# Optimization experiments

Hardware: AMD Instinct MI355X
Metric: run time of the kernel (lower is better)

## Reference

```python
import jax, jax.numpy as jnp
import numpy as np

N = 8192      # total nodes (32 graphs x 256 nodes)
B = 32        # graphs in batch
E = 65536     # edges per graph (avg degree 16)
DK = 512      # d_k = d_v
H = 32        # mlp / conv channel width
VB = 2048     # body visual dim
VF = 512      # face visual dim
EPS = 1e-5


def setup_inputs() -> dict:
    key = jax.random.key(0)
    ks = jax.random.split(key, 26)
    def n(k, sh, s=1.0):
        return jax.random.normal(k, sh, dtype=jnp.float32) * s
    s2, s512, s32 = 1.0 / np.sqrt(2.0), 1.0 / np.sqrt(512.0), 1.0 / np.sqrt(32.0)
    inp = {}
    inp["x"] = n(ks[0], (N, 2))
    inp["visual_body"] = n(ks[1], (N, VB))
    inp["visual_face"] = n(ks[2], (N, VF))
    # attention projections (no bias)
    inp["Wq"] = n(ks[3], (2, DK), s2)
    inp["Wk"] = n(ks[4], (2, DK), s2)
    inp["Wv"] = n(ks[5], (2, DK), s2)
    # input_mlp: LayerNorm(512) -> PReLU -> Linear(512,32)
    inp["ln_g"] = jnp.ones((DK,), jnp.float32)
    inp["ln_b"] = jnp.zeros((DK,), jnp.float32)
    inp["prelu_a"] = jnp.float32(0.25)
    inp["mlp_W"] = n(ks[6], (DK, H), s512)
    inp["mlp_b"] = jnp.zeros((H,), jnp.float32)
    # node projection Linear(32,1)
    inp["np_W"] = n(ks[7], (H, 1), s32)
    inp["np_b"] = jnp.zeros((1,), jnp.float32)
    # CMCosConv linear weights (32->32) for body / face
    inp["body_W"] = n(ks[8], (H, H), s32)
    inp["body_b"] = jnp.zeros((H,), jnp.float32)
    inp["face_W"] = n(ks[9], (H, H), s32)
    inp["face_b"] = jnp.zeros((H,), jnp.float32)
    # gcn projections Linear(32,1)
    inp["pb_W"] = n(ks[10], (H, 1), s32)
    inp["pb_b"] = jnp.zeros((1,), jnp.float32)
    inp["pf_W"] = n(ks[11], (H, 1), s32)
    inp["pf_b"] = jnp.zeros((1,), jnp.float32)
    # int-valued graph structure
    inp["edge_index_body"] = jax.random.randint(ks[12], (2, E), 0, N)
    inp["edge_index_face"] = jax.random.randint(ks[13], (2, E), 0, N)
    inp["batch_vec"] = jnp.arange(N, dtype=jnp.int64) // (N // B)  # 32 graphs, 256 nodes each
    return inp


def cmcos_conv(x, edge_index, visual, W, b):
    # per-edge cosine(visual_src, visual_dst) * Linear(x_src), scatter-sum to dst
    src, dst = edge_index[0], edge_index[1]
    h = x @ W + b                                          # [N, H]
    vn = visual * jax.lax.rsqrt(jnp.sum(visual * visual, -1, keepdims=True) + 1e-8)
    w = jnp.sum(vn[src] * vn[dst], axis=-1)                # [E] cosine edge weights
    msg = w[:, None] * h[src]                              # [E, H]
    return jax.ops.segment_sum(msg, dst, num_segments=x.shape[0])


def reference(x, visual_body, visual_face, Wq, Wk, Wv, ln_g, ln_b, prelu_a,
              mlp_W, mlp_b, np_W, np_b, body_W, body_b, face_W, face_b,
              pb_W, pb_b, pf_W, pf_b, edge_index_body, edge_index_face, batch_vec):
    sz_b = int(batch_vec[-1]) + 1
    q = (x @ Wq).reshape(sz_b, -1, DK)
    k = (x @ Wk).reshape(sz_b, -1, DK)
    v = (x @ Wv).reshape(sz_b, -1, DK)
    attn = jax.nn.softmax(jnp.einsum('bqd,bkd->bqk', q, k) / np.sqrt(DK), axis=-1)
    out = jnp.einsum('bqk,bkd->bqd', attn, v).reshape(-1, DK)   # [N, 512]
    # input_mlp: LayerNorm -> PReLU -> Linear (dropout is identity in eval)
    mu = jnp.mean(out, -1, keepdims=True)
    var = jnp.mean((out - mu) ** 2, -1, keepdims=True)
    h = (out - mu) * jax.lax.rsqrt(var + EPS) * ln_g + ln_b
    h = jnp.where(h >= 0, h, prelu_a * h)
    h = h @ mlp_W + mlp_b                                       # [N, 32]
    nodes_scores = (h @ np_W + np_b)[:, 0]
    hb = cmcos_conv(h, edge_index_body, visual_body, body_W, body_b)
    hf = cmcos_conv(h, edge_index_face, visual_face, face_W, face_b)
    gcn_scores_body = (hb @ pb_W + pb_b)[:, 0]
    gcn_scores_face = (hf @ pf_W + pf_b)[:, 0]
    return nodes_scores + gcn_scores_body + gcn_scores_face
```

## Files before the change

kernel.cpp:

```cpp
#include <hip/hip_runtime.h>

#define NN 8192
#define NB 32
#define NG 256
#define NE 65536
#define DK 512
#define HC 32
#define DB 2048
#define DF 512

#define BODY_DW (NN*DB/4)
#define FACE_DW (NN*DF/4)
#define B_BODY (BODY_DW/2048)
#define B_FACE (FACE_DW/2048)
#define B_FILL 512
#define SLOTS  40
#define QSCALE 16.0f

typedef float v4f __attribute__((ext_vector_type(4)));

#if __has_builtin(__builtin_amdgcn_sdot4)
#define HW_SDOT 1
#else
#define HW_SDOT 0
#endif

__device__ __forceinline__ unsigned pack4_i8(float4 v) {
    const float M = 12582912.0f;
    unsigned b0 = __float_as_uint(fmaf(v.x, QSCALE, M));
    unsigned b1 = __float_as_uint(fmaf(v.y, QSCALE, M));
    unsigned b2 = __float_as_uint(fmaf(v.z, QSCALE, M));
    unsigned b3 = __float_as_uint(fmaf(v.w, QSCALE, M));
    return (b0 & 255u) | ((b1 & 255u) << 8) | ((b2 & 255u) << 16) | ((b3 & 255u) << 24);
}
__device__ __forceinline__ int sdot4(int a, int b, int c) {
#if HW_SDOT
    return __builtin_amdgcn_sdot4(a, b, c, false);
#else
    c += (int)(signed char)(a)       * (int)(signed char)(b);
    c += (int)(signed char)(a >> 8)  * (int)(signed char)(b >> 8);
    c += (int)(signed char)(a >> 16) * (int)(signed char)(b >> 16);
    c += (int)(signed char)(a >> 24) * (int)(signed char)(b >> 24);
    return c;
#endif
}
__device__ __forceinline__ int dot16(int4 a, int4 b, int c) {
    c = sdot4(a.x, b.x, c);
    c = sdot4(a.y, b.y, c);
    c = sdot4(a.z, b.z, c);
    c = sdot4(a.w, b.w, c);
    return c;
}
__device__ __forceinline__ float d4(float4 v) {
    return v.x*v.x + v.y*v.y + v.z*v.z + v.w*v.w;
}
__device__ __forceinline__ v4f prelu4(v4f nd, float alpha) {
    v4f r;
    r.x = (nd.x >= 0.f) ? nd.x : alpha*nd.x;
    r.y = (nd.y >= 0.f) ? nd.y : alpha*nd.y;
    r.z = (nd.z >= 0.f) ? nd.z : alpha*nd.z;
    r.w = (nd.w >= 0.f) ? nd.w : alpha*nd.w;
    return r;
}

struct Params {
    const float *vb, *vf, *x, *Wq, *Wk, *Wv, *ln_g, *ln_b, *prelu_a;
    const float *mlp_W, *mlp_b, *np_W, *np_b, *body_W, *body_b, *face_W, *face_b;
    const float *pb_W, *pb_b, *pf_W, *pf_b;
    const int *eib, *eif;
    unsigned *vnb, *vnf;
    float *invb, *invf;
    float *a_ws, *cb, *cf, *fused;
    float *mvec;
    int *counts, *bkt;
    float *out;
};

__global__ __launch_bounds__(256) void k1_kernel(Params p) {
    __shared__ float2 xs[NG];
    __shared__ float pm[4][4];
    __shared__ float sm4[4];
    __shared__ float rss[16];
    __shared__ float wred[4][8];
    __shared__ float fs_np[HC], fs_fb[HC], fs_ff[HC];
    const int bid = blockIdx.x, tid = threadIdx.x;
    const int lane = tid & 63, wave = tid >> 6;

    if (bid < NB) {
        const int gg = bid;
        xs[tid] = ((const float2*)p.x)[gg*NG + tid];
        const int d = tid * 2;
        float q0a = p.Wq[d],    q0b = p.Wq[d+1];
        float q1a = p.Wq[DK+d], q1b = p.Wq[DK+d+1];
        float k0a = p.Wk[d],    k0b = p.Wk[d+1];
        float k1a = p.Wk[DK+d], k1b = p.Wk[DK+d+1];
        float m00 = q0a*k0a + q0b*k0b;
        float m01 = q0a*k1a + q0b*k1b;
        float m10 = q1a*k0a + q1b*k0b;
        float m11 = q1a*k1a + q1b*k1b;
        #pragma unroll
        for (int off = 32; off > 0; off >>= 1) {
            m00 += __shfl_down(m00,off); m01 += __shfl_down(m01,off);
            m10 += __shfl_down(m10,off); m11 += __shfl_down(m11,off);
        }
        if (lane == 0) { pm[wave][0]=m00; pm[wave][1]=m01; pm[wave][2]=m10; pm[wave][3]=m11; }
        __syncthreads();
        if (tid < 4) sm4[tid] = pm[0][tid] + pm[1][tid] + pm[2][tid] + pm[3][tid];
        __syncthreads();
        const float scale = 0.04419417382415922f;
        const float2 xi = xs[tid];
        const float u0 = (xi.x*sm4[0] + xi.y*sm4[2]) * scale;
        const float u1 = (xi.x*sm4[1] + xi.y*sm4[3]) * scale;
        float m = -1e30f;
        for (int j = 0; j < NG; j++) m = fmaxf(m, u0*xs[j].x + u1*xs[j].y);
        float S = 0.f, a0 = 0.f, a1 = 0.f;
        for (int j = 0; j < NG; j++) {
            float2 xj = xs[j];
            float pr = __expf(u0*xj.x + u1*xj.y - m);
            S += pr; a0 += pr*xj.x; a1 += pr*xj.y;
        }
        const float invS = 1.f / S;
        ((float2*)p.a_ws)[gg*NG + tid] = make_float2(a0*invS, a1*invS);
        return;
    }
    if (bid == NB) {
        {
            const int d = tid * 2;
            float u0 = p.Wv[d], u1 = p.Wv[d+1];
            float w0 = p.Wv[DK+d], w1 = p.Wv[DK+d+1];
            float s0 = u0 + u1, s1 = w0 + w1;
            float q00 = u0*u0 + u1*u1, q01 = u0*w0 + u1*w1, q11 = w0*w0 + w1*w1;
            #pragma unroll
            for (int off = 1; off < 64; off <<= 1) {
                s0 += __shfl_xor(s0,off); s1 += __shfl_xor(s1,off);
                q00 += __shfl_xor(q00,off); q01 += __shfl_xor(q01,off); q11 += __shfl_xor(q11,off);
            }
            if (lane == 0) {
                wred[wave][0]=s0; wred[wave][1]=s1; wred[wave][2]=q00; wred[wave][3]=q01; wred[wave][4]=q11;
            }
        }
        if (tid < HC) {
            float sB = 0.f, sF = 0.f;
            #pragma unroll 8
            for (int c = 0; c < HC; c++) {
                sB += p.body_W[tid*HC + c] * p.pb_W[c];
                sF += p.face_W[tid*HC + c] * p.pf_W[c];
            }
            fs_fb[tid] = sB; fs_ff[tid] = sF;
            fs_np[tid] = p.np_W[tid];
        } else if (tid == HC) {
            float s = 0.f;
            for (int c = 0; c < HC; c++) s += p.body_b[c] * p.pb_W[c];
            p.fused[64] = s;
        } else if (tid == HC + 1) {
            float s = 0.f;
            for (int c = 0; c < HC; c++) s += p.face_b[c] * p.pf_W[c];
            p.fused[65] = s;
        }
        __syncthreads();
        if (tid < 5) p.fused[66+tid] = wred[0][tid]+wred[1][tid]+wred[2][tid]+wred[3][tid];
        #pragma unroll
        for (int rr = tid; rr < DK; rr += 256) {
            const float* row = p.mlp_W + rr*HC;
            float dnp = 0.f, db = 0.f, df = 0.f;
            #pragma unroll 8
            for (int c = 0; c < HC; c++) {
                float w = row[c];
                dnp += w * fs_np[c]; db += w * fs_fb[c]; df += w * fs_ff[c];
            }
            p.mvec[rr] = dnp; p.mvec[DK + rr] = db; p.mvec[2*DK + rr] = df;
        }
        if (tid < 3) {
            const float* fv = (tid == 0) ? fs_np : (tid == 1) ? fs_fb : fs_ff;
            float s = 0.f;
            for (int c = 0; c < HC; c++) s += p.mlp_b[c] * fv[c];
            p.mvec[3*DK + tid] = s;
        }
        return;
    }
    if (bid == NB + 1) {
        int4 z = {0, 0, 0, 0};
        int4* c4 = (int4*)p.counts;
        #pragma unroll
        for (int i = 0; i < (2*NN/4)/256; i++) c4[i*256 + tid] = z;
        return;
    }
    {
        const int pb = bid - (NB + 2);
        const bool body = pb < B_BODY;
        const float4* __restrict__ src = body ? (const float4*)p.vb : (const float4*)p.vf;
        unsigned* __restrict__ dst = body ? p.vnb : p.vnf;
        const int base = (body ? pb : pb - B_BODY) * 2048 + tid;
        if (tid < 16) rss[tid] = 0.f;
        __syncthreads();
        float4 v0 = src[base];
        float4 v1 = src[base + 256];
        float4 v2 = src[base + 512];
        float4 v3 = src[base + 768];
        float4 v4 = src[base + 1024];
        float4 v5 = src[base + 1280];
        float4 v6 = src[base + 1536];
        float4 v7 = src[base + 1792];
        __builtin_amdgcn_sched_barrier(0);
        dst[base]        = pack4_i8(v0);
        dst[base + 256]  = pack4_i8(v1);
        dst[base + 512]  = pack4_i8(v2);
        dst[base + 768]  = pack4_i8(v3);
        dst[base + 1024] = pack4_i8(v4);
        dst[base + 1280] = pack4_i8(v5);
        dst[base + 1536] = pack4_i8(v6);
        dst[base + 1792] = pack4_i8(v7);
        if (body) {
            float sq[4];
            sq[0] = d4(v0) + d4(v1);
            sq[1] = d4(v2) + d4(v3);
            sq[2] = d4(v4) + d4(v5);
            sq[3] = d4(v6) + d4(v7);
            #pragma unroll
            for (int r = 0; r < 4; r++) {
                float ss = sq[r];
                #pragma unroll
                for (int off = 32; off > 0; off >>= 1) ss += __shfl_xor(ss, off);
                if (lane == 0) atomicAdd(&rss[r], ss);
            }
            __syncthreads();
            if (tid < 4) p.invb[pb*4 + tid] = rsqrtf(rss[tid] + 1e-8f);
        } else {
            float sq[8] = {d4(v0), d4(v1), d4(v2), d4(v3), d4(v4), d4(v5), d4(v6), d4(v7)};
            #pragma unroll
            for (int j = 0; j < 8; j++) {
                float ss = sq[j];
                #pragma unroll
                for (int off = 32; off > 0; off >>= 1) ss += __shfl_xor(ss, off);
                if (lane == 0) atomicAdd(&rss[(wave >> 1) + 2*j], ss);
            }
            __syncthreads();
            if (tid < 16) p.invf[(pb - B_BODY)*16 + tid] = rsqrtf(rss[tid] + 1e-8f);
        }
    }
}

__global__ __launch_bounds__(256) void k2_kernel(Params p) {
    const int bid = blockIdx.x, tid = threadIdx.x;
    const int wave = tid >> 6, lane = tid & 63;

    if (bid < B_FILL) {
        const int e = bid * 256 + tid;
        if (e < NE) {
            int s = p.eib[e], d = p.eib[NE + e];
            int slot = atomicAdd(&p.counts[d], 1);
            if (slot < SLOTS) p.bkt[d*SLOTS + slot] = s;
        } else {
            int e2 = e - NE;
            int s = p.eif[e2], d = p.eif[NE + e2];
            int slot = atomicAdd(&p.counts[NN + d], 1);
            if (slot < SLOTS) p.bkt[(NN + d)*SLOTS + slot] = s;
        }
        return;
    }
    const int node = (bid - B_FILL) * 4 + wave;
    const float a0 = p.a_ws[node*2], a1 = p.a_ws[node*2+1];
    const float s0 = p.fused[66], s1 = p.fused[67];
    const float q00 = p.fused[68], q01 = p.fused[69], q11 = p.fused[70];
    const float mean = (a0*s0 + a1*s1) * (1.f/DK);
    const float msq  = (a0*a0*q00 + 2.f*a0*a1*q01 + a1*a1*q11) * (1.f/DK);
    const float inv  = rsqrtf(msq - mean*mean + 1e-5f);
    const float alpha = p.prelu_a[0];

    const v4f* wv0 = (const v4f*)p.Wv;
    const v4f* wv1 = (const v4f*)(p.Wv + DK);
    const v4f* g4 = (const v4f*)p.ln_g;
    const v4f* b4 = (const v4f*)p.ln_b;
    const v4f* mnp = (const v4f*)p.mvec;
    const v4f* mb  = (const v4f*)(p.mvec + DK);
    const v4f* mf  = (const v4f*)(p.mvec + 2*DK);

    const int c4 = lane * 2;
    v4f t0 = prelu4((a0*wv0[c4]   + a1*wv1[c4]   - mean) * inv * g4[c4]   + b4[c4],   alpha);
    v4f t1 = prelu4((a0*wv0[c4+1] + a1*wv1[c4+1] - mean) * inv * g4[c4+1] + b4[c4+1], alpha);

    v4f q0 = t0*mnp[c4] + t1*mnp[c4+1];
    v4f q1 = t0*mb[c4]  + t1*mb[c4+1];
    v4f q2 = t0*mf[c4]  + t1*mf[c4+1];
    float d0 = (q0.x+q0.y) + (q0.z+q0.w);
    float d1 = (q1.x+q1.y) + (q1.z+q1.w);
    float d2 = (q2.x+q2.y) + (q2.z+q2.w);
    #pragma unroll
    for (int off = 1; off < 64; off <<= 1) {
        d0 += __shfl_xor(d0, off);
        d1 += __shfl_xor(d1, off);
        d2 += __shfl_xor(d2, off);
    }
    if (lane == 0) {
        const float qinv2 = 1.0f / (QSCALE * QSCALE);
        p.out[node] = d0 + p.mvec[3*DK] + p.np_b[0] + p.pb_b[0] + p.pf_b[0];
        p.cb[node] = (d1 + p.mvec[3*DK+1] + p.fused[64]) * qinv2 * p.invb[node];
        p.cf[node] = (d2 + p.mvec[3*DK+2] + p.fused[65]) * qinv2 * p.invf[node];
    }
}

__global__ __launch_bounds__(256) void scat_kernel(Params p) {
    const int wave = threadIdx.x >> 6, lane = threadIdx.x & 63;
    const bool body = blockIdx.x < NN/4;
    const int node = (body ? blockIdx.x : blockIdx.x - NN/4) * 4 + wave;
    float acc = 0.f;
    if (body) {
        const int cnt = min(p.counts[node], SLOTS);
        const int* bkt = p.bkt + node*SLOTS;
        const int4* D = (const int4*)(p.vnb + (size_t)node * (DB/4));
        int4 d0 = D[lane], d1 = D[lane + 64];
        for (int i = 0; i < cnt; i += 4) {
            const int4 bi = *(const int4*)(bkt + i);
            const int sA = bi.x;
            const int sB = (i+1 < cnt) ? bi.y : node;
            const int sC = (i+2 < cnt) ? bi.z : node;
            const int sD = (i+3 < cnt) ? bi.w : node;
            const float cA = p.cb[sA];
            const float cB = (i+1 < cnt) ? p.cb[sB] : 0.f;
            const float cC = (i+2 < cnt) ? p.cb[sC] : 0.f;
            const float cD = (i+3 < cnt) ? p.cb[sD] : 0.f;
            const int4* A0 = (const int4*)(p.vnb + (size_t)sA * (DB/4));
            const int4* A1 = (const int4*)(p.vnb + (size_t)sB * (DB/4));
            const int4* A2 = (const int4*)(p.vnb + (size_t)sC * (DB/4));
            const int4* A3 = (const int4*)(p.vnb + (size_t)sD * (DB/4));
            int4 a00 = A0[lane], a01 = A0[lane + 64];
            int4 a10 = A1[lane], a11 = A1[lane + 64];
            int4 a20 = A2[lane], a21 = A2[lane + 64];
            int4 a30 = A3[lane], a31 = A3[lane + 64];
            __builtin_amdgcn_sched_barrier(0);
            int x0 = dot16(a01, d1, dot16(a00, d0, 0));
            int x1 = dot16(a11, d1, dot16(a10, d0, 0));
            int x2 = dot16(a21, d1, dot16(a20, d0, 0));
            int x3 = dot16(a31, d1, dot16(a30, d0, 0));
            acc += (float)x0*cA + (float)x1*cB + (float)x2*cC + (float)x3*cD;
        }
        #pragma unroll
        for (int off = 1; off < 64; off <<= 1) acc += __shfl_xor(acc, off);
        if (lane == 0) atomicAdd(&p.out[node], acc * p.invb[node]);
    } else {
        const int cnt = min(p.counts[NN + node], SLOTS);
        const int* bkt = p.bkt + (size_t)(NN + node)*SLOTS;
        const int2* D = (const int2*)(p.vnf + (size_t)node * (DF/4));
        int2 dd = D[lane];
        for (int i = 0; i < cnt; i += 4) {
            const int4 bi = *(const int4*)(bkt + i);
            const int sA = bi.x;
            const int sB = (i+1 < cnt) ? bi.y : node;
            const int sC = (i+2 < cnt) ? bi.z : node;
            const int sD = (i+3 < cnt) ? bi.w : node;
            const float cA = p.cf[sA];
            const float cB = (i+1 < cnt) ? p.cf[sB] : 0.f;
            const float cC = (i+2 < cnt) ? p.cf[sC] : 0.f;
            const float cD = (i+3 < cnt) ? p.cf[sD] : 0.f;
            const int2* A0 = (const int2*)(p.vnf + (size_t)sA * (DF/4));
            const int2* A1 = (const int2*)(p.vnf + (size_t)sB * (DF/4));
            const int2* A2 = (const int2*)(p.vnf + (size_t)sC * (DF/4));
            const int2* A3 = (const int2*)(p.vnf + (size_t)sD * (DF/4));
            int2 a0 = A0[lane];
            int2 a1 = A1[lane];
            int2 a2 = A2[lane];
            int2 a3 = A3[lane];
            __builtin_amdgcn_sched_barrier(0);
            int x0 = sdot4(a0.y, dd.y, sdot4(a0.x, dd.x, 0));
            int x1 = sdot4(a1.y, dd.y, sdot4(a1.x, dd.x, 0));
            int x2 = sdot4(a2.y, dd.y, sdot4(a2.x, dd.x, 0));
            int x3 = sdot4(a3.y, dd.y, sdot4(a3.x, dd.x, 0));
            acc += (float)x0*cA + (float)x1*cB + (float)x2*cC + (float)x3*cD;
        }
        #pragma unroll
        for (int off = 1; off < 64; off <<= 1) acc += __shfl_xor(acc, off);
        if (lane == 0) atomicAdd(&p.out[node], acc * p.invf[node]);
    }
}

extern "C" void kernel_launch(void* const* d_in, const int* in_sizes, int n_in,
                              void* d_out, int out_size, void* d_ws, size_t ws_size,
                              hipStream_t stream) {
    char* ws = (char*)d_ws;
    size_t off = 0;
    auto alloc = [&](size_t bytes) { void* pp = ws + off; off += (bytes + 15) & ~size_t(15); return pp; };

    Params p;
    p.vb      = (const float*)d_in[1];
    p.vf      = (const float*)d_in[2];
    p.x       = (const float*)d_in[0];
    p.Wq      = (const float*)d_in[3];
    p.Wk      = (const float*)d_in[4];
    p.Wv      = (const float*)d_in[5];
    p.ln_g    = (const float*)d_in[6];
    p.ln_b    = (const float*)d_in[7];
    p.prelu_a = (const float*)d_in[8];
    p.mlp_W   = (const float*)d_in[9];
    p.mlp_b   = (const float*)d_in[10];
    p.np_W    = (const float*)d_in[11];
    p.np_b    = (const float*)d_in[12];
    p.body_W  = (const float*)d_in[13];
    p.body_b  = (const float*)d_in[14];
    p.face_W  = (const float*)d_in[15];
    p.face_b  = (const float*)d_in[16];
    p.pb_W    = (const float*)d_in[17];
    p.pb_b    = (const float*)d_in[18];
    p.pf_W    = (const float*)d_in[19];
    p.pf_b    = (const float*)d_in[20];
    p.eib     = (const int*)d_in[21];
    p.eif     = (const int*)d_in[22];
    p.vnb     = (unsigned*)alloc((size_t)BODY_DW*4);
    p.vnf     = (unsigned*)alloc((size_t)FACE_DW*4);
    p.invb    = (float*)alloc((size_t)NN*4);
    p.invf    = (float*)alloc((size_t)NN*4);
    p.a_ws    = (float*)alloc((size_t)NN*2*4);
    p.cb      = (float*)alloc((size_t)NN*4);
    p.cf      = (float*)alloc((size_t)NN*4);
    p.fused   = (float*)alloc((size_t)72*4);
    p.mvec    = (float*)alloc((size_t)1544*4);
    p.counts  = (int*)alloc((size_t)2*NN*4);
    p.bkt     = (int*)alloc((size_t)2*NN*SLOTS*4);
    p.out     = (float*)d_out;

    k1_kernel<<<NB + 2 + B_BODY + B_FACE, 256, 0, stream>>>(p);
    k2_kernel<<<B_FILL + NN/4, 256, 0, stream>>>(p);
    scat_kernel<<<NN/2, 256, 0, stream>>>(p);
}
```

Baseline: 191.6 us.

## Move edge bucketing into k1 and compute row norms from quantized int8 values

```diff
diff --git a/kernel.cpp b/kernel.cpp
--- a/kernel.cpp
+++ b/kernel.cpp
@@ -50,9 +50,6 @@
     c = sdot4(a.z, b.z, c);
     c = sdot4(a.w, b.w, c);
     return c;
-}
-__device__ __forceinline__ float d4(float4 v) {
-    return v.x*v.x + v.y*v.y + v.z*v.z + v.w*v.w;
 }
 __device__ __forceinline__ v4f prelu4(v4f nd, float alpha) {
     v4f r;
@@ -80,7 +77,7 @@
     __shared__ float2 xs[NG];
     __shared__ float pm[4][4];
     __shared__ float sm4[4];
-    __shared__ float rss[16];
+    __shared__ int rss[16];
     __shared__ float wred[4][8];
     __shared__ float fs_np[HC], fs_fb[HC], fs_ff[HC];
     const int bid = blockIdx.x, tid = threadIdx.x;
@@ -178,20 +175,27 @@
         }
         return;
     }
-    if (bid == NB + 1) {
-        int4 z = {0, 0, 0, 0};
-        int4* c4 = (int4*)p.counts;
-        #pragma unroll
-        for (int i = 0; i < (2*NN/4)/256; i++) c4[i*256 + tid] = z;
+    if (bid < NB + 1 + B_FILL) {
+        const int e = (bid - (NB + 1)) * 256 + tid;
+        if (e < NE) {
+            int s = p.eib[e], d = p.eib[NE + e];
+            int slot = atomicAdd(&p.counts[d], 1);
+            if (slot < SLOTS) p.bkt[d*SLOTS + slot] = s;
+        } else {
+            int e2 = e - NE;
+            int s = p.eif[e2], d = p.eif[NE + e2];
+            int slot = atomicAdd(&p.counts[NN + d], 1);
+            if (slot < SLOTS) p.bkt[(NN + d)*SLOTS + slot] = s;
+        }
         return;
     }
     {
-        const int pb = bid - (NB + 2);
+        const int pb = bid - (NB + 1 + B_FILL);
         const bool body = pb < B_BODY;
         const float4* __restrict__ src = body ? (const float4*)p.vb : (const float4*)p.vf;
         unsigned* __restrict__ dst = body ? p.vnb : p.vnf;
         const int base = (body ? pb : pb - B_BODY) * 2048 + tid;
-        if (tid < 16) rss[tid] = 0.f;
+        if (tid < 16) rss[tid] = 0;
         __syncthreads();
         float4 v0 = src[base];
         float4 v1 = src[base + 256];
@@ -202,63 +206,60 @@
         float4 v6 = src[base + 1536];
         float4 v7 = src[base + 1792];
         __builtin_amdgcn_sched_barrier(0);
-        dst[base]        = pack4_i8(v0);
-        dst[base + 256]  = pack4_i8(v1);
-        dst[base + 512]  = pack4_i8(v2);
-        dst[base + 768]  = pack4_i8(v3);
-        dst[base + 1024] = pack4_i8(v4);
-        dst[base + 1280] = pack4_i8(v5);
-        dst[base + 1536] = pack4_i8(v6);
-        dst[base + 1792] = pack4_i8(v7);
+        unsigned q0 = pack4_i8(v0);
+        unsigned q1 = pack4_i8(v1);
+        unsigned q2 = pack4_i8(v2);
+        unsigned q3 = pack4_i8(v3);
+        unsigned q4 = pack4_i8(v4);
+        unsigned q5 = pack4_i8(v5);
+        unsigned q6 = pack4_i8(v6);
+        unsigned q7 = pack4_i8(v7);
+        dst[base]        = q0;
+        dst[base + 256]  = q1;
+        dst[base + 512]  = q2;
+        dst[base + 768]  = q3;
+        dst[base + 1024] = q4;
+        dst[base + 1280] = q5;
+        dst[base + 1536] = q6;
+        dst[base + 1792] = q7;
         if (body) {
-            float sq[4];
-            sq[0] = d4(v0) + d4(v1);
-            sq[1] = d4(v2) + d4(v3);
-            sq[2] = d4(v4) + d4(v5);
-            sq[3] = d4(v6) + d4(v7);
+            int sq[4];
+            sq[0] = sdot4((int)q1, (int)q1, sdot4((int)q0, (int)q0, 0));
+            sq[1] = sdot4((int)q3, (int)q3, sdot4((int)q2, (int)q2, 0));
+            sq[2] = sdot4((int)q5, (int)q5, sdot4((int)q4, (int)q4, 0));
+            sq[3] = sdot4((int)q7, (int)q7, sdot4((int)q6, (int)q6, 0));
             #pragma unroll
             for (int r = 0; r < 4; r++) {
-                float ss = sq[r];
+                int ss = sq[r];
                 #pragma unroll
                 for (int off = 32; off > 0; off >>= 1) ss += __shfl_xor(ss, off);
                 if (lane == 0) atomicAdd(&rss[r], ss);
             }
             __syncthreads();
-            if (tid < 4) p.invb[pb*4 + tid] = rsqrtf(rss[tid] + 1e-8f);
+            if (tid < 4) p.invb[pb*4 + tid] = rsqrtf((float)rss[tid] + 1.0f);
         } else {
-            float sq[8] = {d4(v0), d4(v1), d4(v2), d4(v3), d4(v4), d4(v5), d4(v6), d4(v7)};
+            int sq[8] = {sdot4((int)q0,(int)q0,0), sdot4((int)q1,(int)q1,0),
+                         sdot4((int)q2,(int)q2,0), sdot4((int)q3,(int)q3,0),
+                         sdot4((int)q4,(int)q4,0), sdot4((int)q5,(int)q5,0),
+                         sdot4((int)q6,(int)q6,0), sdot4((int)q7,(int)q7,0)};
             #pragma unroll
             for (int j = 0; j < 8; j++) {
-                float ss = sq[j];
+                int ss = sq[j];
                 #pragma unroll
                 for (int off = 32; off > 0; off >>= 1) ss += __shfl_xor(ss, off);
                 if (lane == 0) atomicAdd(&rss[(wave >> 1) + 2*j], ss);
             }
             __syncthreads();
-            if (tid < 16) p.invf[(pb - B_BODY)*16 + tid] = rsqrtf(rss[tid] + 1e-8f);
+            if (tid < 16) p.invf[(pb - B_BODY)*16 + tid] = rsqrtf((float)rss[tid] + 1.0f);
         }
     }
 }
 
 __global__ __launch_bounds__(256) void k2_kernel(Params p) {
-    const int bid = blockIdx.x, tid = threadIdx.x;
+    const int tid = threadIdx.x;
     const int wave = tid >> 6, lane = tid & 63;
-
-    if (bid < B_FILL) {
-        const int e = bid * 256 + tid;
-        if (e < NE) {
-            int s = p.eib[e], d = p.eib[NE + e];
-            int slot = atomicAdd(&p.counts[d], 1);
-            if (slot < SLOTS) p.bkt[d*SLOTS + slot] = s;
-        } else {
-            int e2 = e - NE;
-            int s = p.eif[e2], d = p.eif[NE + e2];
-            int slot = atomicAdd(&p.counts[NN + d], 1);
-            if (slot < SLOTS) p.bkt[(NN + d)*SLOTS + slot] = s;
-        }
-        return;
-    }
-    const int node = (bid - B_FILL) * 4 + wave;
+    const int node = blockIdx.x * 4 + wave;
+
     const float a0 = p.a_ws[node*2], a1 = p.a_ws[node*2+1];
     const float s0 = p.fused[66], s1 = p.fused[67];
     const float q00 = p.fused[68], q01 = p.fused[69], q11 = p.fused[70];
@@ -279,12 +280,12 @@
     v4f t0 = prelu4((a0*wv0[c4]   + a1*wv1[c4]   - mean) * inv * g4[c4]   + b4[c4],   alpha);
     v4f t1 = prelu4((a0*wv0[c4+1] + a1*wv1[c4+1] - mean) * inv * g4[c4+1] + b4[c4+1], alpha);
 
-    v4f q0 = t0*mnp[c4] + t1*mnp[c4+1];
-    v4f q1 = t0*mb[c4]  + t1*mb[c4+1];
-    v4f q2 = t0*mf[c4]  + t1*mf[c4+1];
-    float d0 = (q0.x+q0.y) + (q0.z+q0.w);
-    float d1 = (q1.x+q1.y) + (q1.z+q1.w);
-    float d2 = (q2.x+q2.y) + (q2.z+q2.w);
+    v4f w0 = t0*mnp[c4] + t1*mnp[c4+1];
+    v4f w1 = t0*mb[c4]  + t1*mb[c4+1];
+    v4f w2 = t0*mf[c4]  + t1*mf[c4+1];
+    float d0 = (w0.x+w0.y) + (w0.z+w0.w);
+    float d1 = (w1.x+w1.y) + (w1.z+w1.w);
+    float d2 = (w2.x+w2.y) + (w2.z+w2.w);
     #pragma unroll
     for (int off = 1; off < 64; off <<= 1) {
         d0 += __shfl_xor(d0, off);
@@ -292,10 +293,9 @@
         d2 += __shfl_xor(d2, off);
     }
     if (lane == 0) {
-        const float qinv2 = 1.0f / (QSCALE * QSCALE);
         p.out[node] = d0 + p.mvec[3*DK] + p.np_b[0] + p.pb_b[0] + p.pf_b[0];
-        p.cb[node] = (d1 + p.mvec[3*DK+1] + p.fused[64]) * qinv2 * p.invb[node];
-        p.cf[node] = (d2 + p.mvec[3*DK+2] + p.fused[65]) * qinv2 * p.invf[node];
+        p.cb[node] = (d1 + p.mvec[3*DK+1] + p.fused[64]) * p.invb[node];
+        p.cf[node] = (d2 + p.mvec[3*DK+2] + p.fused[65]) * p.invf[node];
     }
 }
 
@@ -417,7 +417,8 @@
     p.bkt     = (int*)alloc((size_t)2*NN*SLOTS*4);
     p.out     = (float*)d_out;
 
-    k1_kernel<<<NB + 2 + B_BODY + B_FACE, 256, 0, stream>>>(p);
-    k2_kernel<<<B_FILL + NN/4, 256, 0, stream>>>(p);
+    hipMemsetAsync(p.counts, 0, (size_t)2*NN*4, stream);
+    k1_kernel<<<NB + 1 + B_FILL + B_BODY + B_FACE, 256, 0, stream>>>(p);
+    k2_kernel<<<NN/4, 256, 0, stream>>>(p);
     scat_kernel<<<NN/2, 256, 0, stream>>>(p);
 }
```

New measurement: 191.3 us. Within noise of the previous version (-0.2%).
